# Kernel tuning notes

Hardware: AMD Instinct MI355X
Metric: run time of the kernel (lower is better)

Reference implementation:

```python
import jax, jax.numpy as jnp
import numpy as np

B, T, V, H, L = 128, 512, 256, 512, 2  # batch, seq, vocab, hidden, layers


def setup_inputs() -> dict:
    key = jax.random.key(0)
    ks = jax.random.split(key, 12)
    s = 0.05
    p = lambda k, shape: (jax.random.normal(k, shape, jnp.float32) * s)
    return {
        "x": jax.random.normal(ks[0], (B, T, V), jnp.float32),
        # layer 0 (input size V)
        "w_ih0": p(ks[1], (4 * H, V)),
        "w_hh0": p(ks[2], (4 * H, H)),
        "b_ih0": p(ks[3], (4 * H,)),
        "b_hh0": p(ks[4], (4 * H,)),
        # layer 1 (input size H)
        "w_ih1": p(ks[5], (4 * H, H)),
        "w_hh1": p(ks[6], (4 * H, H)),
        "b_ih1": p(ks[7], (4 * H,)),
        "b_hh1": p(ks[8], (4 * H,)),
        # final projection
        "fc_w": p(ks[9], (V, H)),
        "fc_b": p(ks[10], (V,)),
    }


def _lstm_layer(x, w_ih, w_hh, b_ih, b_hh):
    """x: [B,T,in] -> (outputs [B,T,H], h_T [B,H], c_T [B,H]). PyTorch gate order i,f,g,o."""
    Bb = x.shape[0]
    Hh = w_hh.shape[1]
    # precompute input contribution for all timesteps: [B,T,4H]
    pre = jnp.einsum('bti,gi->btg', x, w_ih) + b_ih + b_hh

    def step(carry, xt):
        h, c = carry
        gates = xt + h @ w_hh.T  # [B,4H]
        i, f, g, o = jnp.split(gates, 4, axis=-1)
        i = jax.nn.sigmoid(i)
        f = jax.nn.sigmoid(f)
        g = jnp.tanh(g)
        o = jax.nn.sigmoid(o)
        c = f * c + i * g
        h = o * jnp.tanh(c)
        return (h, c), h

    h0 = jnp.zeros((Bb, Hh), x.dtype)
    (hT, cT), hs = jax.lax.scan(step, (h0, h0), jnp.swapaxes(pre, 0, 1))
    return jnp.swapaxes(hs, 0, 1), hT, cT


def reference(x, w_ih0, w_hh0, b_ih0, b_hh0, w_ih1, w_hh1, b_ih1, b_hh1, fc_w, fc_b):
    out0, h0, c0 = _lstm_layer(x, w_ih0, w_hh0, b_ih0, b_hh0)
    out1, h1, c1 = _lstm_layer(out0, w_ih1, w_hh1, b_ih1, b_hh1)
    last = out1[:, -1, :]                # slice final timestep [B,H]
    # dropout is identity in eval mode
    logits = last @ fc_w.T + fc_b        # [B,V]
    h_n = jnp.stack([h0, h1])            # [L,B,H]
    c_n = jnp.stack([c0, c1])
    return (logits, h_n, c_n)
```

## Files before the change

kernel.cpp:

```cpp
#include <hip/hip_runtime.h>
#include <math.h>

#define B_ 128
#define T_ 512
#define V_ 256
#define H_ 512
#define RING_ 64

typedef unsigned short u16;
typedef unsigned int u32;
typedef unsigned long long u64;
typedef __attribute__((ext_vector_type(8))) __bf16 bf16x8;
typedef __attribute__((ext_vector_type(4))) float f32x4;
typedef __attribute__((ext_vector_type(4))) u32 u32x4;

__device__ __forceinline__ float sigf(float x) { return 1.f / (1.f + __expf(-x)); }
__device__ __forceinline__ float tanh_fast(float x) {
    x = fminf(fmaxf(x, -15.f), 15.f);
    float e = __expf(2.f * x);
    return (e - 1.f) / (e + 1.f);
}
__device__ __forceinline__ u16 f2bf(float f) {
    union { float f; u32 u; } v; v.f = f;
    u32 r = v.u + 0x7FFFu + ((v.u >> 16) & 1u);
    return (u16)(r >> 16);
}

__device__ __forceinline__ u64 aload(const u64* p) {
    return __hip_atomic_load(p, __ATOMIC_RELAXED, __HIP_MEMORY_SCOPE_AGENT);
}
__device__ __forceinline__ void astore(u64* p, u64 v) {
    __hip_atomic_store(p, v, __ATOMIC_RELAXED, __HIP_MEMORY_SCOPE_AGENT);
}
__device__ __forceinline__ u32 aload32(const u32* p) {
    return __hip_atomic_load(p, __ATOMIC_RELAXED, __HIP_MEMORY_SCOPE_AGENT);
}
__device__ __forceinline__ void astore32(u32* p, u32 v) {
    __hip_atomic_store(p, v, __ATOMIC_RELAXED, __HIP_MEMORY_SCOPE_AGENT);
}
__device__ __forceinline__ void pollge(const u32* slots, int idx, int target) {
    const u32* p = slots + idx;
    for (;;) {
        u32 v = aload32(p);
        if (__all((int)v >= target)) break;
        __builtin_amdgcn_s_sleep(1);
    }
    __builtin_amdgcn_sched_barrier(0);
    asm volatile("" ::: "memory");
}
__device__ __forceinline__ bf16x8 afrag(const u16* p) {
    union { u64 d[2]; bf16x8 v; } u;
    u.d[0] = aload((const u64*)p);
    u.d[1] = aload((const u64*)(p + 4));
    return u.v;
}

__global__ __launch_bounds__(256) void conv_x(u16* __restrict__ dst, const float* __restrict__ x) {
    int tid = blockIdx.x * 256 + threadIdx.x;
    int k = tid & (V_ - 1);
    int t = (tid >> 8) & (T_ - 1);
    int b = tid >> 17;
    float v = x[tid];
    int lane = (b & 15) | (((k >> 3) & 3) << 4);
    dst[((((size_t)t * 8 + (b >> 4)) * 8) + (k >> 5)) * 512 + (size_t)lane * 8 + (k & 7)] = f2bf(v);
}

__global__ __launch_bounds__(256) void conv_w(u16* __restrict__ dst,
                                              const float* __restrict__ wih,
                                              const float* __restrict__ whh,
                                              int KIN, int Ktot) {
    int tid = blockIdx.x * 256 + threadIdx.x;
    int n = tid / Ktot, k = tid - n * Ktot;
    float v = (k < KIN) ? wih[(size_t)n * KIN + k] : whh[(size_t)n * H_ + (k - KIN)];
    int lane = (n & 15) | (((k >> 3) & 3) << 4);
    dst[((size_t)((n >> 4) * (Ktot >> 5) + (k >> 5))) * 512 + (size_t)lane * 8 + (k & 7)] = f2bf(v);
}

__global__ __launch_bounds__(256) void vadd(float* __restrict__ d,
                                            const float* __restrict__ a,
                                            const float* __restrict__ b, int n) {
    int i = blockIdx.x * 256 + threadIdx.x;
    if (i < n) d[i] = a[i] + b[i];
}


template <int LAYER>
__device__ __forceinline__ void run_loop(
    const u16* __restrict__ Xswz, u16* __restrict__ Out0,
    const u16* __restrict__ WBs,
    f32x4* __restrict__ scr,
    u16* __restrict__ tileb,
    u32* __restrict__ Hgrp,
    const float* __restrict__ bsum, float* __restrict__ out,
    u32* __restrict__ bc,
    int js, int mq, int wid, int lane)
{
    constexpr int KCA = LAYER ? 16 : 8;
    constexpr int KCT = KCA + 16;
    const int m = wid & 1;
    const bool isA = wid < 2;
    const int jl = (js << 4) | (lane & 15);

    if (isA) {
        for (int s = -1; s < T_; ++s) {
            const int tc = s + 1;
            if (tc < T_) {
                f32x4 acc[4];
                #pragma unroll
                for (int g = 0; g < 4; ++g) acc[g] = (f32x4){0.f, 0.f, 0.f, 0.f};
                if (LAYER == 0) {
                    const u16* As = Xswz + (size_t)tc * 32768 + (size_t)(2 * mq + m) * 4096 + (size_t)lane * 8;
                    #pragma unroll
                    for (int kc = 0; kc < 8; ++kc) {
                        bf16x8 a = *(const bf16x8*)(As + (size_t)kc * 512);
                        #pragma unroll
                        for (int g = 0; g < 4; ++g)
                            acc[g] = __builtin_amdgcn_mfma_f32_16x16x32_bf16(
                                a, *(const bf16x8*)(WBs + (size_t)(g * KCT + kc) * 512 + (size_t)lane * 8), acc[g], 0, 0, 0);
                    }
                } else {
                    pollge(bc + m * 32, lane & 31, tc + 1);
                    const u16* As = Out0 + (size_t)tc * 65536 + (size_t)(2 * mq + m) * 8192 + (size_t)lane * 8;
                    bf16x8 fa[16];
                    #pragma unroll
                    for (int kc = 0; kc < 16; ++kc) fa[kc] = afrag(As + (size_t)kc * 512);
                    #pragma unroll
                    for (int kc = 0; kc < 16; ++kc) {
                        #pragma unroll
                        for (int g = 0; g < 4; ++g)
                            acc[g] = __builtin_amdgcn_mfma_f32_16x16x32_bf16(
                                fa[kc], *(const bf16x8*)(WBs + (size_t)(g * KCT + kc) * 512 + (size_t)lane * 8), acc[g], 0, 0, 0);
                    }
                }
                #pragma unroll
                for (int g = 0; g < 4; ++g) scr[(size_t)(((tc & 1) * 2 + m) * 4 + g) * 64 + lane] = acc[g];
            }
            __syncthreads();
        }
    } else {
        const float bi0 = bsum[jl], bi1 = bsum[512 + jl];
        const float bi2 = bsum[1024 + jl], bi3 = bsum[1536 + jl];
        f32x4 creg = {0.f, 0.f, 0.f, 0.f};
        u32* bcs = bc + m * 32 + js;

        for (int s = -1; s < T_; ++s) {
            if (s >= 0) {
                const u32 tag = (u32)s;
                const u32* hb = Hgrp + (size_t)(s & (RING_ - 1)) * 16384 + (size_t)m * 8192;

                f32x4 acc[4];
                #pragma unroll
                for (int g = 0; g < 4; ++g) acc[g] = scr[(size_t)(((s & 1) * 2 + m) * 4 + g) * 64 + lane];

                u32x4 vA[8], vB[8];
                #pragma unroll
                for (int i = 0; i < 8; ++i)
                    vA[i] = *(const u32x4*)(hb + (size_t)(i >> 1) * 512 + (size_t)lane * 8 + (size_t)(i & 1) * 4);

                #pragma unroll
                for (int c = 0; c < 4; ++c) {
                    u32x4* cur = (c & 1) ? vB : vA;
                    u32x4* nxt = (c & 1) ? vA : vB;
                    if (c < 3) {
                        #pragma unroll
                        for (int i = 0; i < 8; ++i)
                            nxt[i] = *(const u32x4*)(hb + (size_t)((c + 1) * 4 + (i >> 1)) * 512 + (size_t)lane * 8 + (size_t)(i & 1) * 4);
                    }
                    u32 bad = 0u;
                    #pragma unroll
                    for (int i = 0; i < 8; ++i)
                        bad |= ((cur[i][0] >> 16) ^ tag) | ((cur[i][1] >> 16) ^ tag)
                             | ((cur[i][2] >> 16) ^ tag) | ((cur[i][3] >> 16) ^ tag);
                    if (__any(bad != 0u)) {
                        for (;;) {
                            #pragma unroll
                            for (int i = 0; i < 8; ++i) {
                                const u64* p = (const u64*)(hb + (size_t)(c * 4 + (i >> 1)) * 512
                                                            + (size_t)lane * 8 + (size_t)(i & 1) * 4);
                                u64 lo = aload(p), hi = aload(p + 1);
                                cur[i][0] = (u32)lo; cur[i][1] = (u32)(lo >> 32);
                                cur[i][2] = (u32)hi; cur[i][3] = (u32)(hi >> 32);
                            }
                            u32 b2 = 0u;
                            #pragma unroll
                            for (int i = 0; i < 8; ++i)
                                b2 |= ((cur[i][0] >> 16) ^ tag) | ((cur[i][1] >> 16) ^ tag)
                                    | ((cur[i][2] >> 16) ^ tag) | ((cur[i][3] >> 16) ^ tag);
                            if (!__any(b2 != 0u)) break;
                            __builtin_amdgcn_s_sleep(1);
                        }
                    }
                    #pragma unroll
                    for (int k2 = 0; k2 < 4; ++k2) {
                        u32x4 a0 = cur[2 * k2], a1 = cur[2 * k2 + 1];
                        u32 w0 = (a0[0] & 0xFFFFu) | (a0[1] << 16);
                        u32 w1 = (a0[2] & 0xFFFFu) | (a0[3] << 16);
                        u32 w2 = (a1[0] & 0xFFFFu) | (a1[1] << 16);
                        u32 w3 = (a1[2] & 0xFFFFu) | (a1[3] << 16);
                        u32x4 ww = {w0, w1, w2, w3};
                        bf16x8 a = __builtin_bit_cast(bf16x8, ww);
                        const int kc = 4 * c + k2;
                        #pragma unroll
                        for (int g = 0; g < 4; ++g)
                            acc[g] = __builtin_amdgcn_mfma_f32_16x16x32_bf16(
                                a, *(const bf16x8*)(WBs + (size_t)(g * KCT + KCA + kc) * 512 + (size_t)lane * 8), acc[g], 0, 0, 0);
                    }
                }

                if (LAYER == 0 && s >= 1 && lane == 0) astore32(bcs, (u32)s);

                const bool is_last = (s == T_ - 1);
                const int bb = (lane >> 4) << 2;
                #pragma unroll
                for (int r = 0; r < 4; ++r) {
                    const float vi = sigf(acc[0][r] + bi0);
                    const float vf = sigf(acc[1][r] + bi1);
                    const float vg = tanh_fast(acc[2][r] + bi2);
                    const float vo = sigf(acc[3][r] + bi3);
                    const float cn = vf * creg[r] + vi * vg;
                    creg[r] = cn;
                    const float hn = vo * tanh_fast(cn);
                    tileb[(size_t)(m * 16 + bb + r) * 20 + (lane & 15)] = f2bf(hn);
                    if (is_last) {
                        const int bg = mq * 32 + m * 16 + bb + r;
                        out[(LAYER ? 98304 : 32768) + bg * 512 + jl] = hn;
                        out[(LAYER ? 229376 : 163840) + bg * 512 + jl] = cn;
                    }
                }
                const u32 wtag = (u32)(s + 1);
                u32* hw = Hgrp + (size_t)((s + 1) & (RING_ - 1)) * 16384 + (size_t)m * 8192;
                #pragma unroll
                for (int q = 0; q < 2; ++q) {
                    u32 w = *(const u32*)&tileb[(size_t)(m * 16 + (lane >> 2)) * 20 + q * 8 + (lane & 3) * 2];
                    u64 v = (u64)(w & 0xFFFFu) | ((u64)wtag << 16)
                          | ((u64)(w >> 16) << 32) | ((u64)wtag << 48);
                    astore((u64*)(hw + (size_t)(js >> 1) * 512 + (size_t)((js & 1) * 2 + q) * 128
                                  + (size_t)(lane >> 2) * 8 + (size_t)((lane & 3) * 2)), v);
                }
                if (LAYER == 0) {
                    const int q2 = lane >> 5, lw = lane & 31, b2 = lw >> 1, e4 = (lw & 1) * 4;
                    u64 v = *(const u64*)&tileb[(size_t)(m * 16 + b2) * 20 + q2 * 8 + e4];
                    astore((u64*)(Out0 + (size_t)s * 65536 + (size_t)(2 * mq + m) * 8192
                                  + (size_t)(js >> 1) * 512 + (size_t)((js & 1) * 2 + q2) * 128
                                  + (size_t)b2 * 8 + (size_t)e4), v);
                }
            }
            __syncthreads();
        }
        if (LAYER == 0) {
            asm volatile("s_waitcnt vmcnt(0)" ::: "memory");
            if (lane == 0) astore32(bcs, (u32)(T_ + 1));
        }
    }
}

__global__ __launch_bounds__(256, 1) void lstm_persistent(
    const u16* __restrict__ Xswz, u16* __restrict__ Out0swz,
    const u16* __restrict__ WB0, const u16* __restrict__ WB1,
    const float* __restrict__ bsum0, const float* __restrict__ bsum1,
    u32* __restrict__ Htag, float* __restrict__ out, u32* __restrict__ bc)
{
    __shared__ u16 WBs[4 * 32 * 512];
    __shared__ f32x4 scr[2 * 2 * 4 * 64];
    __shared__ __align__(16) u16 tileb[2 * 16 * 20];

    const int bid = blockIdx.x;
    const int g = bid & 7, js = bid >> 3;
    const int layer = g >> 2, mq = g & 3;
    const int tid = threadIdx.x;
    const int wid = tid >> 6, lane = tid & 63;

    const int KCtot = layer ? 32 : 24;
    const u16* WB = layer ? WB1 : WB0;
    for (int gg = 0; gg < 4; ++gg) {
        const u32x4* s4 = (const u32x4*)(WB + ((size_t)(gg * 32 + js) * KCtot) * 512);
        u32x4* d4 = (u32x4*)(WBs + (size_t)gg * KCtot * 512);
        for (int i = tid; i < KCtot * 64; i += 256) d4[i] = s4[i];
    }
    __syncthreads();

    u32* Hgrp = Htag + (size_t)g * (RING_ * 16384);
    u32* bcg = bc + mq * 64;

    if (layer == 0)
        run_loop<0>(Xswz, Out0swz, WBs, scr, tileb, Hgrp, bsum0, out, bcg, js, mq, wid, lane);
    else
        run_loop<1>(Xswz, Out0swz, WBs, scr, tileb, Hgrp, bsum1, out, bcg, js, mq, wid, lane);
}

__device__ __forceinline__ float dot4_(float4 a, float4 w, float s) {
    s = fmaf(a.x, w.x, s); s = fmaf(a.y, w.y, s);
    s = fmaf(a.z, w.z, s); s = fmaf(a.w, w.w, s);
    return s;
}

__global__ __launch_bounds__(256) void logits_kernel(
    const float* __restrict__ h1, const float* __restrict__ fc_w,
    const float* __restrict__ fc_b, float* __restrict__ out)
{
    __shared__ float hs[H_];
    const int b = blockIdx.x;
    for (int k = threadIdx.x; k < H_; k += 256) hs[k] = h1[(size_t)b * H_ + k];
    __syncthreads();
    const int v = threadIdx.x;
    const float4* wr = reinterpret_cast<const float4*>(fc_w + (size_t)v * H_);
    const float4* hr = reinterpret_cast<const float4*>(hs);
    float s = 0.f;
    #pragma unroll 8
    for (int k = 0; k < H_ / 4; ++k) s = dot4_(hr[k], wr[k], s);
    out[(size_t)b * V_ + v] = s + fc_b[v];
}

extern "C" void kernel_launch(void* const* d_in, const int* in_sizes, int n_in,
                              void* d_out, int out_size, void* d_ws, size_t ws_size,
                              hipStream_t stream) {
    const float* x     = (const float*)d_in[0];
    const float* w_ih0 = (const float*)d_in[1];
    const float* w_hh0 = (const float*)d_in[2];
    const float* b_ih0 = (const float*)d_in[3];
    const float* b_hh0 = (const float*)d_in[4];
    const float* w_ih1 = (const float*)d_in[5];
    const float* w_hh1 = (const float*)d_in[6];
    const float* b_ih1 = (const float*)d_in[7];
    const float* b_hh1 = (const float*)d_in[8];
    const float* fc_w  = (const float*)d_in[9];
    const float* fc_b  = (const float*)d_in[10];
    float* out = (float*)d_out;

    char* p = (char*)d_ws;
    u16* Xswz    = (u16*)p; p += (size_t)512 * 32768 * 2;
    u16* Out0swz = (u16*)p; p += (size_t)512 * 65536 * 2;
    u16* WB0     = (u16*)p; p += (size_t)128 * 24 * 512 * 2;
    u16* WB1     = (u16*)p; p += (size_t)128 * 32 * 512 * 2;
    u32* Htag    = (u32*)p; p += (size_t)8 * RING_ * 16384 * 4;
    float* bsum0 = (float*)p; p += 2048 * 4;
    float* bsum1 = (float*)p; p += 2048 * 4;
    u32* bc      = (u32*)p;  p += 4 * 64 * 4;

    hipMemsetAsync(Htag, 0, (size_t)8 * RING_ * 16384 * 4, stream);
    hipMemsetAsync(bc, 0, 4 * 64 * 4, stream);
    conv_x<<<65536, 256, 0, stream>>>(Xswz, x);
    conv_w<<<(2048 * 768) / 256, 256, 0, stream>>>(WB0, w_ih0, w_hh0, 256, 768);
    conv_w<<<(2048 * 1024) / 256, 256, 0, stream>>>(WB1, w_ih1, w_hh1, 512, 1024);
    vadd<<<8, 256, 0, stream>>>(bsum0, b_ih0, b_hh0, 2048);
    vadd<<<8, 256, 0, stream>>>(bsum1, b_ih1, b_hh1, 2048);

    lstm_persistent<<<256, 256, 0, stream>>>(
        Xswz, Out0swz, WB0, WB1, bsum0, bsum1, Htag, out, bc);

    logits_kernel<<<B_, 256, 0, stream>>>(out + 98304, fc_w, fc_b, out);
}
```

Measured before the change: 2.749 ms.

## Shrink hidden-state exchange ring to double buffer with sc0 loads

Result: no change. 2.767 ms (+0.7%).

```diff
diff --git a/kernel.cpp b/kernel.cpp
--- a/kernel.cpp
+++ b/kernel.cpp
@@ -5,7 +5,6 @@
 #define T_ 512
 #define V_ 256
 #define H_ 512
-#define RING_ 64
 
 typedef unsigned short u16;
 typedef unsigned int u32;
@@ -53,6 +52,11 @@
     u.d[0] = aload((const u64*)p);
     u.d[1] = aload((const u64*)(p + 4));
     return u.v;
+}
+__device__ __forceinline__ u32x4 ld16sc0(const u32* p) {
+    u32x4 r;
+    asm volatile("global_load_dwordx4 %0, %1, off sc0" : "=v"(r) : "v"(p));
+    return r;
 }
 
 __global__ __launch_bounds__(256) void conv_x(u16* __restrict__ dst, const float* __restrict__ x) {
@@ -146,7 +150,7 @@
         for (int s = -1; s < T_; ++s) {
             if (s >= 0) {
                 const u32 tag = (u32)s;
-                const u32* hb = Hgrp + (size_t)(s & (RING_ - 1)) * 16384 + (size_t)m * 8192;
+                const u32* hb = Hgrp + (size_t)(s & 1) * 16384 + (size_t)m * 8192;
 
                 f32x4 acc[4];
                 #pragma unroll
@@ -155,7 +159,7 @@
                 u32x4 vA[8], vB[8];
                 #pragma unroll
                 for (int i = 0; i < 8; ++i)
-                    vA[i] = *(const u32x4*)(hb + (size_t)(i >> 1) * 512 + (size_t)lane * 8 + (size_t)(i & 1) * 4);
+                    vA[i] = ld16sc0(hb + (size_t)(i >> 1) * 512 + (size_t)lane * 8 + (size_t)(i & 1) * 4);
 
                 #pragma unroll
                 for (int c = 0; c < 4; ++c) {
@@ -164,8 +168,13 @@
                     if (c < 3) {
                         #pragma unroll
                         for (int i = 0; i < 8; ++i)
-                            nxt[i] = *(const u32x4*)(hb + (size_t)((c + 1) * 4 + (i >> 1)) * 512 + (size_t)lane * 8 + (size_t)(i & 1) * 4);
-                    }
+                            nxt[i] = ld16sc0(hb + (size_t)((c + 1) * 4 + (i >> 1)) * 512 + (size_t)lane * 8 + (size_t)(i & 1) * 4);
+                        asm volatile("s_waitcnt vmcnt(8)" ::: "memory");
+                    } else {
+                        asm volatile("s_waitcnt vmcnt(0)" ::: "memory");
+                    }
+                    __builtin_amdgcn_sched_barrier(0);
+
                     u32 bad = 0u;
                     #pragma unroll
                     for (int i = 0; i < 8; ++i)
@@ -228,14 +237,16 @@
                     }
                 }
                 const u32 wtag = (u32)(s + 1);
-                u32* hw = Hgrp + (size_t)((s + 1) & (RING_ - 1)) * 16384 + (size_t)m * 8192;
+                u32* hw = Hgrp + (size_t)((s + 1) & 1) * 16384 + (size_t)m * 8192;
                 #pragma unroll
                 for (int q = 0; q < 2; ++q) {
                     u32 w = *(const u32*)&tileb[(size_t)(m * 16 + (lane >> 2)) * 20 + q * 8 + (lane & 3) * 2];
                     u64 v = (u64)(w & 0xFFFFu) | ((u64)wtag << 16)
                           | ((u64)(w >> 16) << 32) | ((u64)wtag << 48);
-                    astore((u64*)(hw + (size_t)(js >> 1) * 512 + (size_t)((js & 1) * 2 + q) * 128
-                                  + (size_t)(lane >> 2) * 8 + (size_t)((lane & 3) * 2)), v);
+                    u64* dst = (u64*)(hw + (size_t)(js >> 1) * 512 + (size_t)((js & 1) * 2 + q) * 128
+                                      + (size_t)(lane >> 2) * 8 + (size_t)((lane & 3) * 2));
+                    *dst = v;
+                    astore(dst, v);
                 }
                 if (LAYER == 0) {
                     const int q2 = lane >> 5, lw = lane & 31, b2 = lw >> 1, e4 = (lw & 1) * 4;
@@ -279,7 +290,7 @@
     }
     __syncthreads();
 
-    u32* Hgrp = Htag + (size_t)g * (RING_ * 16384);
+    u32* Hgrp = Htag + (size_t)g * 32768;
     u32* bcg = bc + mq * 64;
 
     if (layer == 0)
@@ -332,12 +343,12 @@
     u16* Out0swz = (u16*)p; p += (size_t)512 * 65536 * 2;
     u16* WB0     = (u16*)p; p += (size_t)128 * 24 * 512 * 2;
     u16* WB1     = (u16*)p; p += (size_t)128 * 32 * 512 * 2;
-    u32* Htag    = (u32*)p; p += (size_t)8 * RING_ * 16384 * 4;
+    u32* Htag    = (u32*)p; p += (size_t)8 * 32768 * 4;
     float* bsum0 = (float*)p; p += 2048 * 4;
     float* bsum1 = (float*)p; p += 2048 * 4;
     u32* bc      = (u32*)p;  p += 4 * 64 * 4;
 
-    hipMemsetAsync(Htag, 0, (size_t)8 * RING_ * 16384 * 4, stream);
+    hipMemsetAsync(Htag, 0, (size_t)8 * 32768 * 4, stream);
     hipMemsetAsync(bc, 0, 4 * 64 * 4, stream);
     conv_x<<<65536, 256, 0, stream>>>(Xswz, x);
     conv_w<<<(2048 * 768) / 256, 256, 0, stream>>>(WB0, w_ih0, w_hh0, 256, 768);
```
